# Kernel tuning notes

Measured on AMD Instinct MI355X. Metric: run time of the kernel, lower is better.

Reference implementation:

```python
import jax, jax.numpy as jnp
import numpy as np

N, E = 50000, 800000
IN_CH, H, OUT_CH, ED, L = 64, 128, 128, 1, 4


def setup_inputs() -> dict:
    key = jax.random.key(0)
    ks = jax.random.split(key, 24)
    s = 0.02
    inp = {
        'h': jax.random.normal(ks[0], (N, IN_CH), jnp.float32),
        'coords': jax.random.normal(ks[1], (N, 3), jnp.float32),
        'edge_attr': jax.random.normal(ks[2], (E, ED), jnp.float32),
        'emb_in_W': jax.random.normal(ks[3], (IN_CH, H), jnp.float32) * s,
        'emb_in_b': jnp.zeros((H,), jnp.float32),
        'emb_out_W': jax.random.normal(ks[4], (H, OUT_CH), jnp.float32) * s,
        'emb_out_b': jnp.zeros((OUT_CH,), jnp.float32),
        # per-layer stacked params
        'eW1': jax.random.normal(ks[5], (L, 2 * H + 1 + ED, H), jnp.float32) * s,
        'eb1': jnp.zeros((L, H), jnp.float32),
        'eW2': jax.random.normal(ks[6], (L, H, H), jnp.float32) * s,
        'eb2': jnp.zeros((L, H), jnp.float32),
        'cW1': jax.random.normal(ks[7], (L, H, H), jnp.float32) * s,
        'cb1': jnp.zeros((L, H), jnp.float32),
        'cWc': jax.random.normal(ks[8], (L, H, 1), jnp.float32) * 0.001,  # xavier gain=0.001, no bias
        'nW1': jax.random.normal(ks[9], (L, 2 * H, H), jnp.float32) * s,
        'nb1': jnp.zeros((L, H), jnp.float32),
        'nW2': jax.random.normal(ks[10], (L, H, H), jnp.float32) * s,
        'nb2': jnp.zeros((L, H), jnp.float32),
        'edge_index': jax.random.randint(ks[11], (2, E), 0, N, jnp.int32),
    }
    return inp


def _egnn_forward(h, coords, edge_attr, emb_in_W, emb_in_b, emb_out_W, emb_out_b,
                  eW1, eb1, eW2, eb2, cW1, cb1, cWc, nW1, nb1, nW2, nb2, edge_index):
    silu = jax.nn.silu
    row, col = edge_index[0], edge_index[1]  # PyG: j=source=row, i=target=col
    # count of incoming edges per target node, for coords_agg='mean'
    counts = jax.ops.segment_sum(jnp.ones((E,), jnp.float32), col, num_segments=N)
    counts = jnp.maximum(counts, 1.0)[:, None]
    h = h @ emb_in_W + emb_in_b
    for l in range(L):
        coord_diff = coords[row] - coords[col]                       # [E,3]
        dist = jnp.sum(coord_diff * coord_diff, axis=-1, keepdims=True)  # [E,1]
        # message: edge MLP on cat(x_i, x_j, dist, edge_attr)
        edge_in = jnp.concatenate([h[col], h[row], dist, edge_attr], axis=-1)
        ef = silu(edge_in @ eW1[l] + eb1[l])
        ef = silu(ef @ eW2[l] + eb2[l])                               # [E,H]
        cw = silu(ef @ cW1[l] + cb1[l]) @ cWc[l]                      # [E,1]
        coord_upd = coord_diff * cw                                   # [E,3]
        # aggregate to target nodes
        agg_feat = jax.ops.segment_sum(ef, col, num_segments=N)       # [N,H]
        agg_coord = jax.ops.segment_sum(coord_upd, col, num_segments=N) / counts
        # node update (residual)
        node_in = jnp.concatenate([h, agg_feat], axis=-1)
        upd = silu(node_in @ nW1[l] + nb1[l]) @ nW2[l] + nb2[l]
        h = h + upd
        coords = coords + agg_coord
    h = h @ emb_out_W + emb_out_b
    return h, coords


def reference(h, coords, edge_attr, emb_in_W, emb_in_b, emb_out_W, emb_out_b,
              eW1, eb1, eW2, eb2, cW1, cb1, cWc, nW1, nb1, nW2, nb2, edge_index):
    return _egnn_forward(h, coords, edge_attr, emb_in_W, emb_in_b, emb_out_W, emb_out_b,
                         eW1, eb1, eW2, eb2, cW1, cb1, cWc, nW1, nb1, nW2, nb2, edge_index)
```

## Files before the change

kernel.cpp:

```cpp
#include <hip/hip_runtime.h>

constexpr int Nn = 50000;
constexpr int Ee = 800000;
constexpr int EF_STR  = 136;
constexpr int NIN_STR = 264;
constexpr int HIN_STR = 72;
constexpr int NB_SCAN = (Nn + 255) / 256;

typedef short s8v __attribute__((ext_vector_type(8)));
typedef float f4v __attribute__((ext_vector_type(4)));

__device__ __forceinline__ ushort f2bf(float f) {
    uint u = __float_as_uint(f);
    uint r = (u + 0x7FFFu + ((u >> 16) & 1u)) >> 16;
    return (ushort)r;
}
__device__ __forceinline__ ushort f2bf_t(float f) {
    return (ushort)(__float_as_uint(f) >> 16);
}
__device__ __forceinline__ float bf2f(ushort s) {
    return __uint_as_float(((uint)s) << 16);
}
__device__ __forceinline__ float silu_f(float x) {
    return x * __fdividef(1.0f, 1.0f + __expf(-x));
}
__device__ __forceinline__ uint pack2bf_t(float lo, float hi) {
    return __builtin_amdgcn_perm(__float_as_uint(hi), __float_as_uint(lo), 0x07060302u);
}
__device__ __forceinline__ uint pack2bf_r(float lo, float hi) {
    uint a = __float_as_uint(lo) + 0x8000u;
    uint b = __float_as_uint(hi) + 0x8000u;
    return __builtin_amdgcn_perm(b, a, 0x07060302u);
}

__device__ __forceinline__ void swz_one(const float* src, ushort* dst, int K, int lstride, int KC, int idx)
{
    int per = KC * 4096;
    int l = idx / per, r = idx % per;
    int fb = r >> 9, rem = r & 511;
    int lane = rem >> 3, jj = rem & 7;
    int kc = fb >> 3, t = fb & 7;
    int k = kc * 32 + ((lane >> 4) << 3) + jj;
    int n = t * 16 + (lane & 15);
    float v = (k < K) ? src[(size_t)l * lstride + (size_t)k * 128 + n] : 0.0f;
    dst[idx] = f2bf(v);
}
__global__ void __launch_bounds__(256) k_swz_all(
    const float* __restrict__ eW1, const float* __restrict__ eW2, const float* __restrict__ cW1,
    const float* __restrict__ nW1, const float* __restrict__ nW2,
    const float* __restrict__ inW, const float* __restrict__ outW,
    ushort* __restrict__ oT, ushort* __restrict__ oM,
    ushort* __restrict__ o2, ushort* __restrict__ o3,
    ushort* __restrict__ o4, ushort* __restrict__ o5,
    ushort* __restrict__ o6, ushort* __restrict__ o7)
{
    int gid = blockIdx.x * 256 + threadIdx.x;
    if (gid < 65536)       swz_one(eW1,         oT, 128, 33024, 4, gid);
    else if (gid < 131072) swz_one(eW1 + 16384, oM, 128, 33024, 4, gid - 65536);
    else if (gid < 196608) swz_one(eW2, o2, 128, 16384, 4, gid - 131072);
    else if (gid < 262144) swz_one(cW1, o3, 128, 16384, 4, gid - 196608);
    else if (gid < 393216) swz_one(nW1, o4, 256, 32768, 8, gid - 262144);
    else if (gid < 458752) swz_one(nW2, o5, 128, 16384, 4, gid - 393216);
    else if (gid < 466944) swz_one(inW, o6, 64, 8192, 2, gid - 458752);
    else if (gid < 483328) swz_one(outW, o7, 128, 16384, 4, gid - 466944);
}

__global__ void __launch_bounds__(256) k_count(const int* __restrict__ eidx, int* __restrict__ ecnt)
{
    int e = blockIdx.x * 256 + threadIdx.x;
    atomicAdd(&ecnt[eidx[Ee + e]], 1);
}

__global__ void __launch_bounds__(256) k_bsum(const int* __restrict__ ecnt, int* __restrict__ bsum)
{
    __shared__ int ws[4];
    int tid = threadIdx.x, lane = tid & 63, w = tid >> 6;
    int i = blockIdx.x * 256 + tid;
    int x = (i < Nn) ? ecnt[i] : 0;
    #pragma unroll
    for (int off = 1; off < 64; off <<= 1) x += __shfl_xor(x, off, 64);
    if (lane == 0) ws[w] = x;
    __syncthreads();
    if (tid == 0) bsum[blockIdx.x] = ws[0] + ws[1] + ws[2] + ws[3];
}
__global__ void __launch_bounds__(256) k_bscan(int* __restrict__ bsum)
{
    __shared__ int ws[4];
    int tid = threadIdx.x, lane = tid & 63, w = tid >> 6;
    int x = (tid < NB_SCAN) ? bsum[tid] : 0;
    int s = x;
    #pragma unroll
    for (int off = 1; off < 64; off <<= 1) {
        int t = __shfl_up(s, off, 64);
        if (lane >= off) s += t;
    }
    if (lane == 63) ws[w] = s;
    __syncthreads();
    if (tid == 0) { int a = 0; for (int k = 0; k < 4; k++) { int t = ws[k]; ws[k] = a; a += t; } }
    __syncthreads();
    int excl = ws[w] + s - x;
    if (tid < NB_SCAN) bsum[tid] = excl;
}
__global__ void __launch_bounds__(256) k_cursor(const int* __restrict__ ecnt,
                                               const int* __restrict__ boff, int* __restrict__ cursor)
{
    __shared__ int ws[4];
    int tid = threadIdx.x, lane = tid & 63, w = tid >> 6;
    int i = blockIdx.x * 256 + tid;
    int x = (i < Nn) ? ecnt[i] : 0;
    int s = x;
    #pragma unroll
    for (int off = 1; off < 64; off <<= 1) {
        int t = __shfl_up(s, off, 64);
        if (lane >= off) s += t;
    }
    if (lane == 63) ws[w] = s;
    __syncthreads();
    if (tid == 0) { int a = 0; for (int k = 0; k < 4; k++) { int t = ws[k]; ws[k] = a; a += t; } }
    __syncthreads();
    int excl = ws[w] + s - x + boff[blockIdx.x];
    if (i < Nn) cursor[i] = excl;
}

__global__ void __launch_bounds__(256) k_scatter(
    const int* __restrict__ eidx, const float* __restrict__ edge_attr,
    int* __restrict__ cursor,
    int* __restrict__ srow, int* __restrict__ scol, float* __restrict__ sattr)
{
    int e = blockIdx.x * 256 + threadIdx.x;
    int r = eidx[e], c = eidx[Ee + e];
    int p = atomicAdd(&cursor[c], 1);
    srow[p] = r; scol[p] = c; sattr[p] = edge_attr[e];
}

__global__ void __launch_bounds__(512, 2) k_emb(
    const float* __restrict__ h_in, const float* __restrict__ coords,
    const ushort* __restrict__ ws_, const float* __restrict__ b,
    float* __restrict__ hbuf, ushort* __restrict__ hbf, float* __restrict__ cbuf)
{
    __shared__ alignas(16) ushort s_h[64 * HIN_STR];
    const int tid = threadIdx.x;
    const int nb = blockIdx.x * 64;
    #pragma unroll
    for (int i = 0; i < 2; i++) {
        int idx = i * 512 + tid;
        int e = idx >> 4, ch = idx & 15;
        int node = nb + e;
        float4 f = make_float4(0.f, 0.f, 0.f, 0.f);
        if (node < Nn) f = *(const float4*)(h_in + (size_t)node * 64 + ch * 4);
        ushort4 u; u.x = f2bf(f.x); u.y = f2bf(f.y); u.z = f2bf(f.z); u.w = f2bf(f.w);
        *(ushort4*)(s_h + e * HIN_STR + ch * 4) = u;
    }
    if (tid < 192) {
        int n = nb + tid / 3, d = tid % 3;
        if (n < Nn) cbuf[n * 3 + d] = coords[n * 3 + d];
    }
    __syncthreads();
    const int lane = tid & 63, wave = tid >> 6;
    const int m = lane & 15, quad = lane >> 4;
    const int ws2 = wave >> 2, wt = wave & 3;
    const int rbase = ws2 * 32;
    f4v acc[2][2];
    #pragma unroll
    for (int nt = 0; nt < 2; nt++) { acc[nt][0] = (f4v){0,0,0,0}; acc[nt][1] = (f4v){0,0,0,0}; }
    const ushort* aBase = ws_ + wt * 1024 + lane * 8;
    #pragma unroll
    for (int kc = 0; kc < 2; kc++) {
        s8v a0 = *(const s8v*)(aBase + kc * 4096);
        s8v a1 = *(const s8v*)(aBase + kc * 4096 + 512);
        #pragma unroll
        for (int nt = 0; nt < 2; nt++) {
            s8v bf = *(const s8v*)(s_h + (rbase + nt * 16 + m) * HIN_STR + kc * 32 + quad * 8);
            acc[nt][0] = __builtin_amdgcn_mfma_f32_16x16x32_bf16(a0, bf, acc[nt][0], 0, 0, 0);
            acc[nt][1] = __builtin_amdgcn_mfma_f32_16x16x32_bf16(a1, bf, acc[nt][1], 0, 0, 0);
        }
    }
    #pragma unroll
    for (int nt = 0; nt < 2; nt++) {
        int node = nb + rbase + nt * 16 + m;
        if (node < Nn) {
            #pragma unroll
            for (int ct = 0; ct < 2; ct++) {
                int colb = (wt * 2 + ct) * 16 + quad * 4;
                float4 bb = *(const float4*)(b + colb);
                float v0 = acc[nt][ct][0] + bb.x;
                float v1 = acc[nt][ct][1] + bb.y;
                float v2 = acc[nt][ct][2] + bb.z;
                float v3 = acc[nt][ct][3] + bb.w;
                *(float4*)(hbuf + (size_t)node * 128 + colb) = make_float4(v0, v1, v2, v3);
                uint2 pk; pk.x = pack2bf_r(v0, v1); pk.y = pack2bf_r(v2, v3);
                *(uint2*)(hbf + (size_t)node * 128 + colb) = pk;
            }
        }
    }
}

__global__ void __launch_bounds__(512, 2) k_uv(
    const ushort* __restrict__ hbf,
    const ushort* __restrict__ topW, const ushort* __restrict__ midW,
    const float* __restrict__ b1, ushort* __restrict__ uvb)
{
    __shared__ alignas(16) ushort s_h[64 * EF_STR];
    const int tid = threadIdx.x;
    const int nb = blockIdx.x * 64;
    #pragma unroll
    for (int i = 0; i < 2; i++) {
        int idx = i * 512 + tid;
        int e = idx >> 4, ch = idx & 15;
        int node = nb + e;
        uint4 v = make_uint4(0, 0, 0, 0);
        if (node < Nn) v = *(const uint4*)(hbf + (size_t)node * 128 + ch * 8);
        *(uint4*)(s_h + e * EF_STR + ch * 8) = v;
    }
    __syncthreads();
    const int lane = tid & 63, wave = tid >> 6;
    const int m = lane & 15, quad = lane >> 4;
    const int ws2 = wave >> 2, wt = wave & 3;
    const int rbase = ws2 * 32;
    f4v au[2][2], av[2][2];
    #pragma unroll
    for (int ct = 0; ct < 2; ct++) {
        float4 bb = *(const float4*)(b1 + (wt * 2 + ct) * 16 + quad * 4);
        au[0][ct] = (f4v){bb.x, bb.y, bb.z, bb.w};
        au[1][ct] = au[0][ct];
        av[0][ct] = (f4v){0,0,0,0};
        av[1][ct] = (f4v){0,0,0,0};
    }
    const ushort* tBase = topW + wt * 1024 + (size_t)lane * 8;
    const ushort* mBase = midW + wt * 1024 + (size_t)lane * 8;
    #pragma unroll
    for (int kc = 0; kc < 4; kc++) {
        s8v t0 = *(const s8v*)(tBase + kc * 4096);
        s8v t1 = *(const s8v*)(tBase + kc * 4096 + 512);
        s8v m0 = *(const s8v*)(mBase + kc * 4096);
        s8v m1 = *(const s8v*)(mBase + kc * 4096 + 512);
        #pragma unroll
        for (int nt = 0; nt < 2; nt++) {
            s8v bf = *(const s8v*)(s_h + (rbase + nt * 16 + m) * EF_STR + kc * 32 + quad * 8);
            au[nt][0] = __builtin_amdgcn_mfma_f32_16x16x32_bf16(t0, bf, au[nt][0], 0, 0, 0);
            au[nt][1] = __builtin_amdgcn_mfma_f32_16x16x32_bf16(t1, bf, au[nt][1], 0, 0, 0);
            av[nt][0] = __builtin_amdgcn_mfma_f32_16x16x32_bf16(m0, bf, av[nt][0], 0, 0, 0);
            av[nt][1] = __builtin_amdgcn_mfma_f32_16x16x32_bf16(m1, bf, av[nt][1], 0, 0, 0);
        }
    }
    #pragma unroll
    for (int nt = 0; nt < 2; nt++) {
        int node = nb + rbase + nt * 16 + m;
        if (node < Nn) {
            #pragma unroll
            for (int ct = 0; ct < 2; ct++) {
                int colb = (wt * 2 + ct) * 16 + quad * 4;
                uint2 pu; pu.x = pack2bf_r(au[nt][ct][0], au[nt][ct][1]);
                          pu.y = pack2bf_r(au[nt][ct][2], au[nt][ct][3]);
                *(uint2*)(uvb + (size_t)node * 256 + colb) = pu;
                uint2 pv; pv.x = pack2bf_r(av[nt][ct][0], av[nt][ct][1]);
                          pv.y = pack2bf_r(av[nt][ct][2], av[nt][ct][3]);
                *(uint2*)(uvb + (size_t)node * 256 + 128 + colb) = pv;
            }
        }
    }
}

__device__ __forceinline__ uint uv_term(uint uw, uint vw, float dist, float attr,
                                        const float* wdp, const float* wap, int j)
{
    float2 w2d = *(const float2*)(wdp + 2 * j);
    float2 w2a = *(const float2*)(wap + 2 * j);
    float lo = __uint_as_float(uw << 16) + __uint_as_float(vw << 16)
             + dist * w2d.x + attr * w2a.x;
    float hi = __uint_as_float(uw & 0xFFFF0000u) + __uint_as_float(vw & 0xFFFF0000u)
             + dist * w2d.y + attr * w2a.y;
    return pack2bf_t(silu_f(lo), silu_f(hi));
}

__global__ void __launch_bounds__(512, 8) k_edge(
    const float* __restrict__ cbuf,
    const int* __restrict__ srow, const int* __restrict__ scol, const float* __restrict__ sattr,
    const ushort* __restrict__ uvb,
    const float* __restrict__ wd, const float* __restrict__ wa,
    const ushort* __restrict__ w2s, const float* __restrict__ b2,
    const ushort* __restrict__ cw1s, const float* __restrict__ cb1,
    const float* __restrict__ cwc,
    float* __restrict__ agg_feat, float* __restrict__ agg_coord)
{
    __shared__ alignas(16) ushort s_a[128 * EF_STR];
    __shared__ alignas(16) float  s_p[128 * 4];
    __shared__ float s_dist[128];
    __shared__ int   s_col[128];
    __shared__ float s_cd[128 * 3];

    const int tid = threadIdx.x;
    const int eb = blockIdx.x * 128;

    if (tid < 128) {
        int rw = srow[eb + tid], cl = scol[eb + tid];
        s_col[tid] = cl;
        float d0 = cbuf[rw * 3 + 0] - cbuf[cl * 3 + 0];
        float d1 = cbuf[rw * 3 + 1] - cbuf[cl * 3 + 1];
        float d2 = cbuf[rw * 3 + 2] - cbuf[cl * 3 + 2];
        s_cd[tid * 3 + 0] = d0; s_cd[tid * 3 + 1] = d1; s_cd[tid * 3 + 2] = d2;
        s_dist[tid] = d0 * d0 + d1 * d1 + d2 * d2;
    }
    __syncthreads();

    {
        const int e = tid >> 2, ch = tid & 3;
        int row = srow[eb + e], col = scol[eb + e];
        float attr = sattr[eb + e];
        float dist = s_dist[e];
        const ushort* up = uvb + (size_t)col * 256 + ch * 32;
        const ushort* vp = uvb + (size_t)row * 256 + 128 + ch * 32;
        #pragma unroll
        for (int hf = 0; hf < 2; hf++) {
            uint4 ua = *(const uint4*)(up + hf * 16);
            uint4 ub = *(const uint4*)(up + hf * 16 + 8);
            uint4 va = *(const uint4*)(vp + hf * 16);
            uint4 vb = *(const uint4*)(vp + hf * 16 + 8);
            const float* wdp = wd + ch * 32 + hf * 16;
            const float* wap = wa + ch * 32 + hf * 16;
            uint4 q0, q1;
            q0.x = uv_term(ua.x, va.x, dist, attr, wdp, wap, 0);
            q0.y = uv_term(ua.y, va.y, dist, attr, wdp, wap, 1);
            q0.z = uv_term(ua.z, va.z, dist, attr, wdp, wap, 2);
            q0.w = uv_term(ua.w, va.w, dist, attr, wdp, wap, 3);
            *(uint4*)(s_a + e * EF_STR + ch * 32 + hf * 16) = q0;
            q1.x = uv_term(ub.x, vb.x, dist, attr, wdp, wap, 4);
            q1.y = uv_term(ub.y, vb.y, dist, attr, wdp, wap, 5);
            q1.z = uv_term(ub.z, vb.z, dist, attr, wdp, wap, 6);
            q1.w = uv_term(ub.w, vb.w, dist, attr, wdp, wap, 7);
            *(uint4*)(s_a + e * EF_STR + ch * 32 + hf * 16 + 8) = q1;
        }
    }
    __syncthreads();

    const int lane = tid & 63, wave = tid >> 6;
    const int m = lane & 15, quad = lane >> 4;
    const int ws2 = wave >> 2, wt = wave & 3;
    const int rbase = ws2 * 64;

    f4v acc2[4][2];
    {
        #pragma unroll
        for (int tt = 0; tt < 2; tt++) {
            float4 bb = *(const float4*)(b2 + (wt * 2 + tt) * 16 + quad * 4);
            f4v b4 = (f4v){bb.x, bb.y, bb.z, bb.w};
            #pragma unroll
            for (int mt = 0; mt < 4; mt++) acc2[mt][tt] = b4;
        }
        const ushort* bBase = w2s + wt * 1024 + (size_t)lane * 8;
        #pragma unroll
        for (int kc = 0; kc < 4; kc++) {
            s8v b0 = *(const s8v*)(bBase + kc * 4096);
            s8v b1v = *(const s8v*)(bBase + kc * 4096 + 512);
            #pragma unroll
            for (int mt = 0; mt < 4; mt++) {
                s8v a = *(const s8v*)(s_a + (rbase + mt * 16 + m) * EF_STR + kc * 32 + quad * 8);
                acc2[mt][0] = __builtin_amdgcn_mfma_f32_16x16x32_bf16(b0, a, acc2[mt][0], 0, 0, 0);
                acc2[mt][1] = __builtin_amdgcn_mfma_f32_16x16x32_bf16(b1v, a, acc2[mt][1], 0, 0, 0);
            }
        }
    }
    __syncthreads();
    #pragma unroll
    for (int mt = 0; mt < 4; mt++)
        #pragma unroll
        for (int tt = 0; tt < 2; tt++) {
            uint2 pk;
            pk.x = pack2bf_t(silu_f(acc2[mt][tt][0]), silu_f(acc2[mt][tt][1]));
            pk.y = pack2bf_t(silu_f(acc2[mt][tt][2]), silu_f(acc2[mt][tt][3]));
            *(uint2*)(s_a + (rbase + mt * 16 + m) * EF_STR + (wt * 2 + tt) * 16 + quad * 4) = pk;
        }
    __syncthreads();

    {
        f4v acc3[4][2];
        #pragma unroll
        for (int tt = 0; tt < 2; tt++) {
            float4 bb = *(const float4*)(cb1 + (wt * 2 + tt) * 16 + quad * 4);
            f4v b4 = (f4v){bb.x, bb.y, bb.z, bb.w};
            #pragma unroll
            for (int mt = 0; mt < 4; mt++) acc3[mt][tt] = b4;
        }
        const ushort* bBase = cw1s + wt * 1024 + (size_t)lane * 8;
        #pragma unroll
        for (int kc = 0; kc < 4; kc++) {
            s8v b0 = *(const s8v*)(bBase + kc * 4096);
            s8v b1v = *(const s8v*)(bBase + kc * 4096 + 512);
            #pragma unroll
            for (int mt = 0; mt < 4; mt++) {
                s8v a = *(const s8v*)(s_a + (rbase + mt * 16 + m) * EF_STR + kc * 32 + quad * 8);
                acc3[mt][0] = __builtin_amdgcn_mfma_f32_16x16x32_bf16(b0, a, acc3[mt][0], 0, 0, 0);
                acc3[mt][1] = __builtin_amdgcn_mfma_f32_16x16x32_bf16(b1v, a, acc3[mt][1], 0, 0, 0);
            }
        }
        float4 wc0 = *(const float4*)(cwc + (wt * 2 + 0) * 16 + quad * 4);
        float4 wc1 = *(const float4*)(cwc + (wt * 2 + 1) * 16 + quad * 4);
        #pragma unroll
        for (int mt = 0; mt < 4; mt++) {
            float p = silu_f(acc3[mt][0][0]) * wc0.x + silu_f(acc3[mt][0][1]) * wc0.y
                    + silu_f(acc3[mt][0][2]) * wc0.z + silu_f(acc3[mt][0][3]) * wc0.w
                    + silu_f(acc3[mt][1][0]) * wc1.x + silu_f(acc3[mt][1][1]) * wc1.y
                    + silu_f(acc3[mt][1][2]) * wc1.z + silu_f(acc3[mt][1][3]) * wc1.w;
            p += __shfl_xor(p, 16, 64);
            p += __shfl_xor(p, 32, 64);
            if (quad == 0) s_p[(rbase + mt * 16 + m) * 4 + wt] = p;
        }
    }
    __syncthreads();

    if (tid < 128) {
        float4 pt = *(const float4*)(s_p + tid * 4);
        float cw = pt.x + pt.y + pt.z + pt.w;
        int cn = s_col[tid];
        unsafeAtomicAdd(&agg_coord[cn * 3 + 0], s_cd[tid * 3 + 0] * cw);
        unsafeAtomicAdd(&agg_coord[cn * 3 + 1], s_cd[tid * 3 + 1] * cw);
        unsafeAtomicAdd(&agg_coord[cn * 3 + 2], s_cd[tid * 3 + 2] * cw);
    }
    {
        int j = tid & 127;
        int e0 = (tid >> 7) * 32;
        float accv = 0.0f; int cur = s_col[e0];
        #pragma unroll 4
        for (int ee = e0; ee < e0 + 32; ee++) {
            int c = s_col[ee];
            if (c != cur) {
                unsafeAtomicAdd(&agg_feat[(size_t)cur * 128 + j], accv);
                accv = 0.0f; cur = c;
            }
            accv += bf2f(s_a[ee * EF_STR + j]);
        }
        unsafeAtomicAdd(&agg_feat[(size_t)cur * 128 + j], accv);
    }
}

__global__ void __launch_bounds__(512, 6) k_node(
    float* __restrict__ hbuf, ushort* __restrict__ hbf, float* __restrict__ cbuf,
    float* __restrict__ agg_feat, float* __restrict__ agg_coord,
    const int* __restrict__ ecnt,
    const ushort* __restrict__ w1s, const float* __restrict__ b1,
    const ushort* __restrict__ w2s, const float* __restrict__ b2)
{
    __shared__ alignas(16) ushort s_nin[64 * NIN_STR];
    __shared__ alignas(16) ushort s_t1[64 * EF_STR];
    const int tid = threadIdx.x;
    const int nb = blockIdx.x * 64;

    #pragma unroll
    for (int i = 0; i < 2; i++) {
        int idx = i * 512 + tid;
        int e = idx >> 4, ch = idx & 15;
        int node = nb + e;
        uint4 v = make_uint4(0, 0, 0, 0);
        if (node < Nn) v = *(const uint4*)(hbf + (size_t)node * 128 + ch * 8);
        *(uint4*)(s_nin + e * NIN_STR + ch * 8) = v;
    }
    #pragma unroll
    for (int i = 0; i < 4; i++) {
        int idx = i * 512 + tid;
        int e = idx >> 5, ch = idx & 31;
        int node = nb + e;
        float4 f = make_float4(0.f, 0.f, 0.f, 0.f);
        if (node < Nn) {
            f = *(const float4*)(agg_feat + (size_t)node * 128 + ch * 4);
            *(float4*)(agg_feat + (size_t)node * 128 + ch * 4) = make_float4(0.f, 0.f, 0.f, 0.f);
        }
        uint2 pk; pk.x = pack2bf_t(f.x, f.y); pk.y = pack2bf_t(f.z, f.w);
        *(uint2*)(s_nin + e * NIN_STR + 128 + ch * 4) = pk;
    }
    if (tid < 64) {
        int n = nb + tid;
        if (n < Nn) {
            float c = (float)ecnt[n]; c = (c < 1.0f) ? 1.0f : c;
            float inv = __fdividef(1.0f, c);
            cbuf[n * 3 + 0] += agg_coord[n * 3 + 0] * inv;
            cbuf[n * 3 + 1] += agg_coord[n * 3 + 1] * inv;
            cbuf[n * 3 + 2] += agg_coord[n * 3 + 2] * inv;
            agg_coord[n * 3 + 0] = 0.f; agg_coord[n * 3 + 1] = 0.f; agg_coord[n * 3 + 2] = 0.f;
        }
    }
    __syncthreads();

    const int lane = tid & 63, wave = tid >> 6;
    const int m = lane & 15, quad = lane >> 4;
    const int ws2 = wave >> 2, wt = wave & 3;
    const int rbase = ws2 * 32;

    {
        f4v acc[2][2];
        #pragma unroll
        for (int ct = 0; ct < 2; ct++) {
            float4 bb = *(const float4*)(b1 + (wt * 2 + ct) * 16 + quad * 4);
            acc[0][ct] = (f4v){bb.x, bb.y, bb.z, bb.w};
            acc[1][ct] = acc[0][ct];
        }
        const ushort* aBase = w1s + wt * 1024 + (size_t)lane * 8;
        #pragma unroll
        for (int kc = 0; kc < 8; kc++) {
            s8v a0 = *(const s8v*)(aBase + kc * 4096);
            s8v a1 = *(const s8v*)(aBase + kc * 4096 + 512);
            #pragma unroll
            for (int nt = 0; nt < 2; nt++) {
                s8v bf = *(const s8v*)(s_nin + (rbase + nt * 16 + m) * NIN_STR + kc * 32 + quad * 8);
                acc[nt][0] = __builtin_amdgcn_mfma_f32_16x16x32_bf16(a0, bf, acc[nt][0], 0, 0, 0);
                acc[nt][1] = __builtin_amdgcn_mfma_f32_16x16x32_bf16(a1, bf, acc[nt][1], 0, 0, 0);
            }
        }
        #pragma unroll
        for (int nt = 0; nt < 2; nt++) {
            int row = rbase + nt * 16 + m;
            #pragma unroll
            for (int ct = 0; ct < 2; ct++) {
                int colb = (wt * 2 + ct) * 16 + quad * 4;
                float v0 = silu_f(acc[nt][ct][0]);
                float v1 = silu_f(acc[nt][ct][1]);
                float v2 = silu_f(acc[nt][ct][2]);
                float v3 = silu_f(acc[nt][ct][3]);
                uint2 pk; pk.x = pack2bf_t(v0, v1); pk.y = pack2bf_t(v2, v3);
                *(uint2*)(s_t1 + row * EF_STR + colb) = pk;
            }
        }
    }
    __syncthreads();

    {
        f4v acc[2][2];
        #pragma unroll
        for (int ct = 0; ct < 2; ct++) {
            float4 bb = *(const float4*)(b2 + (wt * 2 + ct) * 16 + quad * 4);
            acc[0][ct] = (f4v){bb.x, bb.y, bb.z, bb.w};
            acc[1][ct] = acc[0][ct];
        }
        const ushort* aBase = w2s + wt * 1024 + (size_t)lane * 8;
        #pragma unroll
        for (int kc = 0; kc < 4; kc++) {
            s8v a0 = *(const s8v*)(aBase + kc * 4096);
            s8v a1 = *(const s8v*)(aBase + kc * 4096 + 512);
            #pragma unroll
            for (int nt = 0; nt < 2; nt++) {
                s8v bf = *(const s8v*)(s_t1 + (rbase + nt * 16 + m) * EF_STR + kc * 32 + quad * 8);
                acc[nt][0] = __builtin_amdgcn_mfma_f32_16x16x32_bf16(a0, bf, acc[nt][0], 0, 0, 0);
                acc[nt][1] = __builtin_amdgcn_mfma_f32_16x16x32_bf16(a1, bf, acc[nt][1], 0, 0, 0);
            }
        }
        #pragma unroll
        for (int nt = 0; nt < 2; nt++) {
            int node = nb + rbase + nt * 16 + m;
            if (node < Nn) {
                #pragma unroll
                for (int ct = 0; ct < 2; ct++) {
                    int colb = (wt * 2 + ct) * 16 + quad * 4;
                    float4 old = *(const float4*)(hbuf + (size_t)node * 128 + colb);
                    float v0 = old.x + acc[nt][ct][0];
                    float v1 = old.y + acc[nt][ct][1];
                    float v2 = old.z + acc[nt][ct][2];
                    float v3 = old.w + acc[nt][ct][3];
                    *(float4*)(hbuf + (size_t)node * 128 + colb) = make_float4(v0, v1, v2, v3);
                    uint2 pk; pk.x = pack2bf_r(v0, v1); pk.y = pack2bf_r(v2, v3);
                    *(uint2*)(hbf + (size_t)node * 128 + colb) = pk;
                }
            }
        }
    }
}

__global__ void __launch_bounds__(512, 2) k_emb_out(
    const ushort* __restrict__ hbf, const float* __restrict__ cbuf,
    const ushort* __restrict__ ws_, const float* __restrict__ b, float* __restrict__ out)
{
    __shared__ alignas(16) ushort s_h[64 * EF_STR];
    const int tid = threadIdx.x;
    const int nb = blockIdx.x * 64;
    #pragma unroll
    for (int i = 0; i < 2; i++) {
        int idx = i * 512 + tid;
        int e = idx >> 4, ch = idx & 15;
        int node = nb + e;
        uint4 v = make_uint4(0, 0, 0, 0);
        if (node < Nn) v = *(const uint4*)(hbf + (size_t)node * 128 + ch * 8);
        *(uint4*)(s_h + e * EF_STR + ch * 8) = v;
    }
    if (tid < 192) {
        int n = nb + tid / 3, d = tid % 3;
        if (n < Nn) out[(size_t)Nn * 128 + n * 3 + d] = cbuf[n * 3 + d];
    }
    __syncthreads();
    const int lane = tid & 63, wave = tid >> 6;
    const int m = lane & 15, quad = lane >> 4;
    const int ws2 = wave >> 2, wt = wave & 3;
    const int rbase = ws2 * 32;
    f4v acc[2][2];
    #pragma unroll
    for (int ct = 0; ct < 2; ct++) {
        float4 bb = *(const float4*)(b + (wt * 2 + ct) * 16 + quad * 4);
        acc[0][ct] = (f4v){bb.x, bb.y, bb.z, bb.w};
        acc[1][ct] = acc[0][ct];
    }
    const ushort* aBase = ws_ + wt * 1024 + (size_t)lane * 8;
    #pragma unroll
    for (int kc = 0; kc < 4; kc++) {
        s8v a0 = *(const s8v*)(aBase + kc * 4096);
        s8v a1 = *(const s8v*)(aBase + kc * 4096 + 512);
        #pragma unroll
        for (int nt = 0; nt < 2; nt++) {
            s8v bf = *(const s8v*)(s_h + (rbase + nt * 16 + m) * EF_STR + kc * 32 + quad * 8);
            acc[nt][0] = __builtin_amdgcn_mfma_f32_16x16x32_bf16(a0, bf, acc[nt][0], 0, 0, 0);
            acc[nt][1] = __builtin_amdgcn_mfma_f32_16x16x32_bf16(a1, bf, acc[nt][1], 0, 0, 0);
        }
    }
    #pragma unroll
    for (int nt = 0; nt < 2; nt++) {
        int node = nb + rbase + nt * 16 + m;
        if (node < Nn) {
            #pragma unroll
            for (int ct = 0; ct < 2; ct++) {
                int colb = (wt * 2 + ct) * 16 + quad * 4;
                float4 o = make_float4(acc[nt][ct][0], acc[nt][ct][1],
                                       acc[nt][ct][2], acc[nt][ct][3]);
                *(float4*)(out + (size_t)node * 128 + colb) = o;
            }
        }
    }
}

extern "C" void kernel_launch(void* const* d_in, const int* in_sizes, int n_in,
                              void* d_out, int out_size, void* d_ws, size_t ws_size,
                              hipStream_t stream)
{
    const float* h_in      = (const float*)d_in[0];
    const float* coords    = (const float*)d_in[1];
    const float* edge_attr = (const float*)d_in[2];
    const float* emb_in_W  = (const float*)d_in[3];
    const float* emb_in_b  = (const float*)d_in[4];
    const float* emb_out_W = (const float*)d_in[5];
    const float* emb_out_b = (const float*)d_in[6];
    const float* eW1 = (const float*)d_in[7];
    const float* eb1 = (const float*)d_in[8];
    const float* eW2 = (const float*)d_in[9];
    const float* eb2 = (const float*)d_in[10];
    const float* cW1 = (const float*)d_in[11];
    const float* cb1 = (const float*)d_in[12];
    const float* cWc = (const float*)d_in[13];
    const float* nW1 = (const float*)d_in[14];
    const float* nb1 = (const float*)d_in[15];
    const float* nW2 = (const float*)d_in[16];
    const float* nb2 = (const float*)d_in[17];
    const int*  eidx = (const int*)d_in[18];

    size_t off = 0;
    char* base = (char*)d_ws;
    auto alloc = [&](size_t bytes) -> char* {
        char* p = base + off;
        off += (bytes + 255) & ~(size_t)255;
        return p;
    };
    float*  hbuf      = (float*)alloc((size_t)Nn * 128 * 4);
    ushort* hbf       = (ushort*)alloc((size_t)Nn * 128 * 2);
    ushort* uvb       = (ushort*)alloc((size_t)Nn * 256 * 2);
    float*  cbuf      = (float*)alloc((size_t)Nn * 3 * 4);
    int*    ecnt      = (int*)alloc((size_t)Nn * 4);
    int*    cursor    = (int*)alloc((size_t)Nn * 4);
    int*    bsum      = (int*)alloc((size_t)NB_SCAN * 4);
    int*    srow      = (int*)alloc((size_t)Ee * 4);
    int*    scol      = (int*)alloc((size_t)Ee * 4);
    float*  sattr     = (float*)alloc((size_t)Ee * 4);
    float*  agg_feat  = (float*)alloc((size_t)Nn * 128 * 4);
    float*  agg_coord = (float*)alloc((size_t)Nn * 3 * 4);
    ushort* eW1tops   = (ushort*)alloc((size_t)4 * 16384 * 2);
    ushort* eW1mids   = (ushort*)alloc((size_t)4 * 16384 * 2);
    ushort* eW2s      = (ushort*)alloc((size_t)4 * 16384 * 2);
    ushort* cW1s      = (ushort*)alloc((size_t)4 * 16384 * 2);
    ushort* nW1s      = (ushort*)alloc((size_t)4 * 32768 * 2);
    ushort* nW2s      = (ushort*)alloc((size_t)4 * 16384 * 2);
    ushort* eInWs     = (ushort*)alloc((size_t)8192 * 2);
    ushort* eOutWs    = (ushort*)alloc((size_t)16384 * 2);

    k_swz_all<<<483328 / 256, 256, 0, stream>>>(
        eW1, eW2, cW1, nW1, nW2, emb_in_W, emb_out_W,
        eW1tops, eW1mids, eW2s, cW1s, nW1s, nW2s, eInWs, eOutWs);

    hipMemsetAsync(ecnt, 0, (size_t)Nn * 4, stream);
    k_count<<<Ee / 256, 256, 0, stream>>>(eidx, ecnt);
    k_bsum<<<NB_SCAN, 256, 0, stream>>>(ecnt, bsum);
    k_bscan<<<1, 256, 0, stream>>>(bsum);
    k_cursor<<<NB_SCAN, 256, 0, stream>>>(ecnt, bsum, cursor);
    k_scatter<<<Ee / 256, 256, 0, stream>>>(eidx, edge_attr, cursor, srow, scol, sattr);
    k_emb<<<(Nn + 63) / 64, 512, 0, stream>>>(h_in, coords, eInWs, emb_in_b, hbuf, hbf, cbuf);

    hipMemsetAsync(agg_feat, 0, (size_t)Nn * 128 * 4, stream);
    hipMemsetAsync(agg_coord, 0, (size_t)Nn * 3 * 4, stream);

    for (int l = 0; l < 4; l++) {
        k_uv<<<(Nn + 63) / 64, 512, 0, stream>>>(
            hbf, eW1tops + (size_t)l * 16384, eW1mids + (size_t)l * 16384,
            eb1 + l * 128, uvb);
        k_edge<<<Ee / 128, 512, 0, stream>>>(
            cbuf, srow, scol, sattr, uvb,
            eW1 + ((size_t)l * 258 + 256) * 128,
            eW1 + ((size_t)l * 258 + 257) * 128,
            eW2s + (size_t)l * 16384, eb2 + l * 128,
            cW1s + (size_t)l * 16384, cb1 + l * 128,
            cWc + l * 128,
            agg_feat, agg_coord);
        k_node<<<(Nn + 63) / 64, 512, 0, stream>>>(
            hbuf, hbf, cbuf, agg_feat, agg_coord, ecnt,
            nW1s + (size_t)l * 32768, nb1 + l * 128,
            nW2s + (size_t)l * 16384, nb2 + l * 128);
    }
    k_emb_out<<<(Nn + 63) / 64, 512, 0, stream>>>(hbf, cbuf, eOutWs, emb_out_b, (float*)d_out);
}
```

Before: 1.579 ms.

## Fuse per-layer u/v projection into embedding and node kernels, stage edge weights in LDS

Removes the separate k_uv kernel. The first layer's u/v projection now runs at the end of k_emb, and each later layer's projection runs at the end of the previous k_node, using the freshly computed bf16 h already held in shared memory. This saves a kernel launch and a global re-read of hbf per layer, at the cost of more shared memory and registers in the fused kernels. It also stages the dist/attr weight rows in LDS inside k_edge and raises wave priority around the MFMA loops.

```diff
diff --git a/kernel.cpp b/kernel.cpp
--- a/kernel.cpp
+++ b/kernel.cpp
@@ -136,9 +136,12 @@
 __global__ void __launch_bounds__(512, 2) k_emb(
     const float* __restrict__ h_in, const float* __restrict__ coords,
     const ushort* __restrict__ ws_, const float* __restrict__ b,
-    float* __restrict__ hbuf, ushort* __restrict__ hbf, float* __restrict__ cbuf)
+    float* __restrict__ hbuf, ushort* __restrict__ hbf, float* __restrict__ cbuf,
+    const ushort* __restrict__ topW, const ushort* __restrict__ midW,
+    const float* __restrict__ b1, ushort* __restrict__ uvb)
 {
     __shared__ alignas(16) ushort s_h[64 * HIN_STR];
+    __shared__ alignas(16) ushort s_hb[64 * EF_STR];
     const int tid = threadIdx.x;
     const int nb = blockIdx.x * 64;
     #pragma unroll
@@ -160,102 +163,85 @@
     const int m = lane & 15, quad = lane >> 4;
     const int ws2 = wave >> 2, wt = wave & 3;
     const int rbase = ws2 * 32;
-    f4v acc[2][2];
-    #pragma unroll
-    for (int nt = 0; nt < 2; nt++) { acc[nt][0] = (f4v){0,0,0,0}; acc[nt][1] = (f4v){0,0,0,0}; }
-    const ushort* aBase = ws_ + wt * 1024 + lane * 8;
-    #pragma unroll
-    for (int kc = 0; kc < 2; kc++) {
-        s8v a0 = *(const s8v*)(aBase + kc * 4096);
-        s8v a1 = *(const s8v*)(aBase + kc * 4096 + 512);
+    {
+        f4v acc[2][2];
+        #pragma unroll
+        for (int nt = 0; nt < 2; nt++) { acc[nt][0] = (f4v){0,0,0,0}; acc[nt][1] = (f4v){0,0,0,0}; }
+        const ushort* aBase = ws_ + wt * 1024 + lane * 8;
+        #pragma unroll
+        for (int kc = 0; kc < 2; kc++) {
+            s8v a0 = *(const s8v*)(aBase + kc * 4096);
+            s8v a1 = *(const s8v*)(aBase + kc * 4096 + 512);
+            #pragma unroll
+            for (int nt = 0; nt < 2; nt++) {
+                s8v bf = *(const s8v*)(s_h + (rbase + nt * 16 + m) * HIN_STR + kc * 32 + quad * 8);
+                acc[nt][0] = __builtin_amdgcn_mfma_f32_16x16x32_bf16(a0, bf, acc[nt][0], 0, 0, 0);
+                acc[nt][1] = __builtin_amdgcn_mfma_f32_16x16x32_bf16(a1, bf, acc[nt][1], 0, 0, 0);
+            }
+        }
         #pragma unroll
         for (int nt = 0; nt < 2; nt++) {
-            s8v bf = *(const s8v*)(s_h + (rbase + nt * 16 + m) * HIN_STR + kc * 32 + quad * 8);
-            acc[nt][0] = __builtin_amdgcn_mfma_f32_16x16x32_bf16(a0, bf, acc[nt][0], 0, 0, 0);
-            acc[nt][1] = __builtin_amdgcn_mfma_f32_16x16x32_bf16(a1, bf, acc[nt][1], 0, 0, 0);
-        }
-    }
-    #pragma unroll
-    for (int nt = 0; nt < 2; nt++) {
-        int node = nb + rbase + nt * 16 + m;
-        if (node < Nn) {
+            int node = nb + rbase + nt * 16 + m;
             #pragma unroll
             for (int ct = 0; ct < 2; ct++) {
                 int colb = (wt * 2 + ct) * 16 + quad * 4;
-                float4 bb = *(const float4*)(b + colb);
-                float v0 = acc[nt][ct][0] + bb.x;
-                float v1 = acc[nt][ct][1] + bb.y;
-                float v2 = acc[nt][ct][2] + bb.z;
-                float v3 = acc[nt][ct][3] + bb.w;
-                *(float4*)(hbuf + (size_t)node * 128 + colb) = make_float4(v0, v1, v2, v3);
-                uint2 pk; pk.x = pack2bf_r(v0, v1); pk.y = pack2bf_r(v2, v3);
-                *(uint2*)(hbf + (size_t)node * 128 + colb) = pk;
-            }
-        }
-    }
-}
-
-__global__ void __launch_bounds__(512, 2) k_uv(
-    const ushort* __restrict__ hbf,
-    const ushort* __restrict__ topW, const ushort* __restrict__ midW,
-    const float* __restrict__ b1, ushort* __restrict__ uvb)
-{
-    __shared__ alignas(16) ushort s_h[64 * EF_STR];
-    const int tid = threadIdx.x;
-    const int nb = blockIdx.x * 64;
-    #pragma unroll
-    for (int i = 0; i < 2; i++) {
-        int idx = i * 512 + tid;
-        int e = idx >> 4, ch = idx & 15;
-        int node = nb + e;
-        uint4 v = make_uint4(0, 0, 0, 0);
-        if (node < Nn) v = *(const uint4*)(hbf + (size_t)node * 128 + ch * 8);
-        *(uint4*)(s_h + e * EF_STR + ch * 8) = v;
-    }
-    __syncthreads();
-    const int lane = tid & 63, wave = tid >> 6;
-    const int m = lane & 15, quad = lane >> 4;
-    const int ws2 = wave >> 2, wt = wave & 3;
-    const int rbase = ws2 * 32;
-    f4v au[2][2], av[2][2];
-    #pragma unroll
-    for (int ct = 0; ct < 2; ct++) {
-        float4 bb = *(const float4*)(b1 + (wt * 2 + ct) * 16 + quad * 4);
-        au[0][ct] = (f4v){bb.x, bb.y, bb.z, bb.w};
-        au[1][ct] = au[0][ct];
-        av[0][ct] = (f4v){0,0,0,0};
-        av[1][ct] = (f4v){0,0,0,0};
-    }
-    const ushort* tBase = topW + wt * 1024 + (size_t)lane * 8;
-    const ushort* mBase = midW + wt * 1024 + (size_t)lane * 8;
-    #pragma unroll
-    for (int kc = 0; kc < 4; kc++) {
-        s8v t0 = *(const s8v*)(tBase + kc * 4096);
-        s8v t1 = *(const s8v*)(tBase + kc * 4096 + 512);
-        s8v m0 = *(const s8v*)(mBase + kc * 4096);
-        s8v m1 = *(const s8v*)(mBase + kc * 4096 + 512);
+                uint2 pk = make_uint2(0u, 0u);
+                if (node < Nn) {
+                    float4 bb = *(const float4*)(b + colb);
+                    float v0 = acc[nt][ct][0] + bb.x;
+                    float v1 = acc[nt][ct][1] + bb.y;
+                    float v2 = acc[nt][ct][2] + bb.z;
+                    float v3 = acc[nt][ct][3] + bb.w;
+                    *(float4*)(hbuf + (size_t)node * 128 + colb) = make_float4(v0, v1, v2, v3);
+                    pk.x = pack2bf_r(v0, v1); pk.y = pack2bf_r(v2, v3);
+                    *(uint2*)(hbf + (size_t)node * 128 + colb) = pk;
+                }
+                *(uint2*)(s_hb + (rbase + nt * 16 + m) * EF_STR + colb) = pk;
+            }
+        }
+    }
+    __syncthreads();
+    {
+        f4v au[2][2], av[2][2];
+        #pragma unroll
+        for (int ct = 0; ct < 2; ct++) {
+            float4 bb = *(const float4*)(b1 + (wt * 2 + ct) * 16 + quad * 4);
+            au[0][ct] = (f4v){bb.x, bb.y, bb.z, bb.w};
+            au[1][ct] = au[0][ct];
+            av[0][ct] = (f4v){0,0,0,0};
+            av[1][ct] = (f4v){0,0,0,0};
+        }
+        const ushort* tBase = topW + wt * 1024 + (size_t)lane * 8;
+        const ushort* mBase = midW + wt * 1024 + (size_t)lane * 8;
+        #pragma unroll
+        for (int kc = 0; kc < 4; kc++) {
+            s8v t0 = *(const s8v*)(tBase + kc * 4096);
+            s8v t1 = *(const s8v*)(tBase + kc * 4096 + 512);
+            s8v m0 = *(const s8v*)(mBase + kc * 4096);
+            s8v m1 = *(const s8v*)(mBase + kc * 4096 + 512);
+            #pragma unroll
+            for (int nt = 0; nt < 2; nt++) {
+                s8v bf = *(const s8v*)(s_hb + (rbase + nt * 16 + m) * EF_STR + kc * 32 + quad * 8);
+                au[nt][0] = __builtin_amdgcn_mfma_f32_16x16x32_bf16(t0, bf, au[nt][0], 0, 0, 0);
+                au[nt][1] = __builtin_amdgcn_mfma_f32_16x16x32_bf16(t1, bf, au[nt][1], 0, 0, 0);
+                av[nt][0] = __builtin_amdgcn_mfma_f32_16x16x32_bf16(m0, bf, av[nt][0], 0, 0, 0);
+                av[nt][1] = __builtin_amdgcn_mfma_f32_16x16x32_bf16(m1, bf, av[nt][1], 0, 0, 0);
+            }
+        }
         #pragma unroll
         for (int nt = 0; nt < 2; nt++) {
-            s8v bf = *(const s8v*)(s_h + (rbase + nt * 16 + m) * EF_STR + kc * 32 + quad * 8);
-            au[nt][0] = __builtin_amdgcn_mfma_f32_16x16x32_bf16(t0, bf, au[nt][0], 0, 0, 0);
-            au[nt][1] = __builtin_amdgcn_mfma_f32_16x16x32_bf16(t1, bf, au[nt][1], 0, 0, 0);
-            av[nt][0] = __builtin_amdgcn_mfma_f32_16x16x32_bf16(m0, bf, av[nt][0], 0, 0, 0);
-            av[nt][1] = __builtin_amdgcn_mfma_f32_16x16x32_bf16(m1, bf, av[nt][1], 0, 0, 0);
-        }
-    }
-    #pragma unroll
-    for (int nt = 0; nt < 2; nt++) {
-        int node = nb + rbase + nt * 16 + m;
-        if (node < Nn) {
-            #pragma unroll
-            for (int ct = 0; ct < 2; ct++) {
-                int colb = (wt * 2 + ct) * 16 + quad * 4;
-                uint2 pu; pu.x = pack2bf_r(au[nt][ct][0], au[nt][ct][1]);
-                          pu.y = pack2bf_r(au[nt][ct][2], au[nt][ct][3]);
-                *(uint2*)(uvb + (size_t)node * 256 + colb) = pu;
-                uint2 pv; pv.x = pack2bf_r(av[nt][ct][0], av[nt][ct][1]);
-                          pv.y = pack2bf_r(av[nt][ct][2], av[nt][ct][3]);
-                *(uint2*)(uvb + (size_t)node * 256 + 128 + colb) = pv;
+            int node = nb + rbase + nt * 16 + m;
+            if (node < Nn) {
+                #pragma unroll
+                for (int ct = 0; ct < 2; ct++) {
+                    int colb = (wt * 2 + ct) * 16 + quad * 4;
+                    uint2 pu; pu.x = pack2bf_r(au[nt][ct][0], au[nt][ct][1]);
+                              pu.y = pack2bf_r(au[nt][ct][2], au[nt][ct][3]);
+                    *(uint2*)(uvb + (size_t)node * 256 + colb) = pu;
+                    uint2 pv; pv.x = pack2bf_r(av[nt][ct][0], av[nt][ct][1]);
+                              pv.y = pack2bf_r(av[nt][ct][2], av[nt][ct][3]);
+                    *(uint2*)(uvb + (size_t)node * 256 + 128 + colb) = pv;
+                }
             }
         }
     }
@@ -288,6 +274,8 @@
     __shared__ float s_dist[128];
     __shared__ int   s_col[128];
     __shared__ float s_cd[128 * 3];
+    __shared__ alignas(16) float s_wd[128];
+    __shared__ alignas(16) float s_wa[128];
 
     const int tid = threadIdx.x;
     const int eb = blockIdx.x * 128;
@@ -300,6 +288,10 @@
         float d2 = cbuf[rw * 3 + 2] - cbuf[cl * 3 + 2];
         s_cd[tid * 3 + 0] = d0; s_cd[tid * 3 + 1] = d1; s_cd[tid * 3 + 2] = d2;
         s_dist[tid] = d0 * d0 + d1 * d1 + d2 * d2;
+    } else if (tid < 256) {
+        s_wd[tid - 128] = wd[tid - 128];
+    } else if (tid < 384) {
+        s_wa[tid - 256] = wa[tid - 256];
     }
     __syncthreads();
 
@@ -316,8 +308,8 @@
             uint4 ub = *(const uint4*)(up + hf * 16 + 8);
             uint4 va = *(const uint4*)(vp + hf * 16);
             uint4 vb = *(const uint4*)(vp + hf * 16 + 8);
-            const float* wdp = wd + ch * 32 + hf * 16;
-            const float* wap = wa + ch * 32 + hf * 16;
+            const float* wdp = s_wd + ch * 32 + hf * 16;
+            const float* wap = s_wa + ch * 32 + hf * 16;
             uint4 q0, q1;
             q0.x = uv_term(ua.x, va.x, dist, attr, wdp, wap, 0);
             q0.y = uv_term(ua.y, va.y, dist, attr, wdp, wap, 1);
@@ -348,6 +340,7 @@
             for (int mt = 0; mt < 4; mt++) acc2[mt][tt] = b4;
         }
         const ushort* bBase = w2s + wt * 1024 + (size_t)lane * 8;
+        __builtin_amdgcn_s_setprio(1);
         #pragma unroll
         for (int kc = 0; kc < 4; kc++) {
             s8v b0 = *(const s8v*)(bBase + kc * 4096);
@@ -359,6 +352,7 @@
                 acc2[mt][1] = __builtin_amdgcn_mfma_f32_16x16x32_bf16(b1v, a, acc2[mt][1], 0, 0, 0);
             }
         }
+        __builtin_amdgcn_s_setprio(0);
     }
     __syncthreads();
     #pragma unroll
@@ -382,6 +376,7 @@
             for (int mt = 0; mt < 4; mt++) acc3[mt][tt] = b4;
         }
         const ushort* bBase = cw1s + wt * 1024 + (size_t)lane * 8;
+        __builtin_amdgcn_s_setprio(1);
         #pragma unroll
         for (int kc = 0; kc < 4; kc++) {
             s8v b0 = *(const s8v*)(bBase + kc * 4096);
@@ -393,6 +388,7 @@
                 acc3[mt][1] = __builtin_amdgcn_mfma_f32_16x16x32_bf16(b1v, a, acc3[mt][1], 0, 0, 0);
             }
         }
+        __builtin_amdgcn_s_setprio(0);
         float4 wc0 = *(const float4*)(cwc + (wt * 2 + 0) * 16 + quad * 4);
         float4 wc1 = *(const float4*)(cwc + (wt * 2 + 1) * 16 + quad * 4);
         #pragma unroll
@@ -438,7 +434,9 @@
     float* __restrict__ agg_feat, float* __restrict__ agg_coord,
     const int* __restrict__ ecnt,
     const ushort* __restrict__ w1s, const float* __restrict__ b1,
-    const ushort* __restrict__ w2s, const float* __restrict__ b2)
+    const ushort* __restrict__ w2s, const float* __restrict__ b2,
+    const ushort* __restrict__ topW, const ushort* __restrict__ midW,
+    const float* __restrict__ b1e, ushort* __restrict__ uvb, int do_uv)
 {
     __shared__ alignas(16) ushort s_nin[64 * NIN_STR];
     __shared__ alignas(16) ushort s_t1[64 * EF_STR];
@@ -545,18 +543,67 @@
         #pragma unroll
         for (int nt = 0; nt < 2; nt++) {
             int node = nb + rbase + nt * 16 + m;
-            if (node < Nn) {
-                #pragma unroll
-                for (int ct = 0; ct < 2; ct++) {
-                    int colb = (wt * 2 + ct) * 16 + quad * 4;
+            #pragma unroll
+            for (int ct = 0; ct < 2; ct++) {
+                int colb = (wt * 2 + ct) * 16 + quad * 4;
+                uint2 pk = make_uint2(0u, 0u);
+                if (node < Nn) {
                     float4 old = *(const float4*)(hbuf + (size_t)node * 128 + colb);
                     float v0 = old.x + acc[nt][ct][0];
                     float v1 = old.y + acc[nt][ct][1];
                     float v2 = old.z + acc[nt][ct][2];
                     float v3 = old.w + acc[nt][ct][3];
                     *(float4*)(hbuf + (size_t)node * 128 + colb) = make_float4(v0, v1, v2, v3);
-                    uint2 pk; pk.x = pack2bf_r(v0, v1); pk.y = pack2bf_r(v2, v3);
+                    pk.x = pack2bf_r(v0, v1); pk.y = pack2bf_r(v2, v3);
                     *(uint2*)(hbf + (size_t)node * 128 + colb) = pk;
+                }
+                if (do_uv)
+                    *(uint2*)(s_nin + (rbase + nt * 16 + m) * EF_STR + colb) = pk;
+            }
+        }
+    }
+
+    if (do_uv) {
+        __syncthreads();
+        f4v au[2][2], av[2][2];
+        #pragma unroll
+        for (int ct = 0; ct < 2; ct++) {
+            float4 bb = *(const float4*)(b1e + (wt * 2 + ct) * 16 + quad * 4);
+            au[0][ct] = (f4v){bb.x, bb.y, bb.z, bb.w};
+            au[1][ct] = au[0][ct];
+            av[0][ct] = (f4v){0,0,0,0};
+            av[1][ct] = (f4v){0,0,0,0};
+        }
+        const ushort* tBase = topW + wt * 1024 + (size_t)lane * 8;
+        const ushort* mBase = midW + wt * 1024 + (size_t)lane * 8;
+        #pragma unroll
+        for (int kc = 0; kc < 4; kc++) {
+            s8v t0 = *(const s8v*)(tBase + kc * 4096);
+            s8v t1 = *(const s8v*)(tBase + kc * 4096 + 512);
+            s8v m0 = *(const s8v*)(mBase + kc * 4096);
+            s8v m1 = *(const s8v*)(mBase + kc * 4096 + 512);
+            #pragma unroll
+            for (int nt = 0; nt < 2; nt++) {
+                s8v bf = *(const s8v*)(s_nin + (rbase + nt * 16 + m) * EF_STR + kc * 32 + quad * 8);
+                au[nt][0] = __builtin_amdgcn_mfma_f32_16x16x32_bf16(t0, bf, au[nt][0], 0, 0, 0);
+                au[nt][1] = __builtin_amdgcn_mfma_f32_16x16x32_bf16(t1, bf, au[nt][1], 0, 0, 0);
+                av[nt][0] = __builtin_amdgcn_mfma_f32_16x16x32_bf16(m0, bf, av[nt][0], 0, 0, 0);
+                av[nt][1] = __builtin_amdgcn_mfma_f32_16x16x32_bf16(m1, bf, av[nt][1], 0, 0, 0);
+            }
+        }
+        #pragma unroll
+        for (int nt = 0; nt < 2; nt++) {
+            int node = nb + rbase + nt * 16 + m;
+            if (node < Nn) {
+                #pragma unroll
+                for (int ct = 0; ct < 2; ct++) {
+                    int colb = (wt * 2 + ct) * 16 + quad * 4;
+                    uint2 pu; pu.x = pack2bf_r(au[nt][ct][0], au[nt][ct][1]);
+                              pu.y = pack2bf_r(au[nt][ct][2], au[nt][ct][3]);
+                    *(uint2*)(uvb + (size_t)node * 256 + colb) = pu;
+                    uint2 pv; pv.x = pack2bf_r(av[nt][ct][0], av[nt][ct][1]);
+                              pv.y = pack2bf_r(av[nt][ct][2], av[nt][ct][3]);
+                    *(uint2*)(uvb + (size_t)node * 256 + 128 + colb) = pv;
                 }
             }
         }
@@ -684,15 +731,14 @@
     k_bscan<<<1, 256, 0, stream>>>(bsum);
     k_cursor<<<NB_SCAN, 256, 0, stream>>>(ecnt, bsum, cursor);
     k_scatter<<<Ee / 256, 256, 0, stream>>>(eidx, edge_attr, cursor, srow, scol, sattr);
-    k_emb<<<(Nn + 63) / 64, 512, 0, stream>>>(h_in, coords, eInWs, emb_in_b, hbuf, hbf, cbuf);
+    k_emb<<<(Nn + 63) / 64, 512, 0, stream>>>(
+        h_in, coords, eInWs, emb_in_b, hbuf, hbf, cbuf,
+        eW1tops, eW1mids, eb1, uvb);
 
     hipMemsetAsync(agg_feat, 0, (size_t)Nn * 128 * 4, stream);
     hipMemsetAsync(agg_coord, 0, (size_t)Nn * 3 * 4, stream);
 
     for (int l = 0; l < 4; l++) {
-        k_uv<<<(Nn + 63) / 64, 512, 0, stream>>>(
-            hbf, eW1tops + (size_t)l * 16384, eW1mids + (size_t)l * 16384,
-            eb1 + l * 128, uvb);
         k_edge<<<Ee / 128, 512, 0, stream>>>(
             cbuf, srow, scol, sattr, uvb,
             eW1 + ((size_t)l * 258 + 256) * 128,
@@ -701,10 +747,13 @@
             cW1s + (size_t)l * 16384, cb1 + l * 128,
             cWc + l * 128,
             agg_feat, agg_coord);
+        int ln = (l < 3) ? (l + 1) : 0;
         k_node<<<(Nn + 63) / 64, 512, 0, stream>>>(
             hbuf, hbf, cbuf, agg_feat, agg_coord, ecnt,
             nW1s + (size_t)l * 32768, nb1 + l * 128,
-            nW2s + (size_t)l * 16384, nb2 + l * 128);
+            nW2s + (size_t)l * 16384, nb2 + l * 128,
+            eW1tops + (size_t)ln * 16384, eW1mids + (size_t)ln * 16384,
+            eb1 + ln * 128, uvb, (l < 3) ? 1 : 0);
     }
     k_emb_out<<<(Nn + 63) / 64, 512, 0, stream>>>(hbf, cbuf, eOutWs, emb_out_b, (float*)d_out);
 }
```

After: 1.431 ms. -9.3%, faster.
